# Performance work log

Hardware: AMD Instinct MI355X
Metric: run time of the kernel (lower is better)

## Reference

```python
import jax, jax.numpy as jnp
import numpy as np

B, C = 32768, 1000
ALPHA, P, BETA = 0.5, 2.0, 0.3
E1, E2 = 60, 80
MAGIC = 0.165745444183859  # constant subtracted from max_m in __init__


def setup_inputs() -> dict:
    key = jax.random.key(0)
    k1, k2, k3, k4 = jax.random.split(key, 4)
    x = jax.random.normal(k1, (B, C), dtype=jnp.float32)
    targets = jax.random.randint(k2, (B,), 0, C)
    # per-class sample counts (long-tailed): positive floats in [5, 1280]
    cls_num_list = jax.random.uniform(k3, (C,), dtype=jnp.float32, minval=5.0, maxval=1280.0)
    class_difficulty = jax.random.uniform(k4, (C,), dtype=jnp.float32)
    return {"x": x, "targets": targets, "cls_num_list": cls_num_list,
            "class_difficulty": class_difficulty, "epoch": 70}


def reference(x, targets, cls_num_list, class_difficulty, epoch):
    # ---- margins from class frequency (computed in __init__) ----
    max_m = -jnp.log(jnp.min(cls_num_list) / jnp.sum(cls_num_list)) - MAGIC
    cls_p = 1.0 / jnp.sqrt(cls_num_list)          # [C]
    m_list = max_m * cls_p / jnp.max(cls_p)       # [C]
    # ---- difficulty-based weights ----
    weights = ALPHA * class_difficulty ** P + BETA
    weights = weights * (max_m / jnp.max(weights))
    # ---- epoch schedule (epoch is a static Python int) ----
    if epoch < E1:
        m_list1 = m_list
    else:
        ee = 1.0 if epoch >= E2 else (epoch - E1) / (E2 - E1)
        m_list1 = m_list + weights * ee / 2
    # ---- subtract per-sample margin only at the target logit ----
    batch_m = m_list1[targets]                    # [B], == matmul(m_list1, onehot.T)
    rows = jnp.arange(B)
    output = x.at[rows, targets].add(-batch_m)    # torch.where(index, x - batch_m, x)
    # ---- safe_cross_entropy with s=1.0 (s kwarg not passed at call site) ----
    log_probs = jax.nn.log_softmax(output * 1.0, axis=1)
    loss = -jnp.mean(log_probs[rows, targets])
    return loss
```

## Files before the change

kernel.cpp:

```cpp
#include <hip/hip_runtime.h>
#include <math.h>

#define B_SZ 32768
#define C_SZ 1000
#define NV4  250

typedef float fvec4 __attribute__((ext_vector_type(4)));

__constant__ float kMAGIC = 0.165745444183859f;

__global__ void prep_kernel(const float* __restrict__ cls,
                            const float* __restrict__ diff,
                            const int*   __restrict__ epoch_p,
                            float*       __restrict__ m1) {
    __shared__ float smin[256], ssum[256], smax[256];
    const int tid = threadIdx.x;
    float mn = INFINITY, sm = 0.f, mx = -INFINITY;
    for (int c = tid; c < C_SZ; c += 256) {
        float v = cls[c];
        mn = fminf(mn, v);
        sm += v;
        mx = fmaxf(mx, diff[c]);
    }
    smin[tid] = mn; ssum[tid] = sm; smax[tid] = mx;
    __syncthreads();
    for (int s = 128; s > 0; s >>= 1) {
        if (tid < s) {
            smin[tid] = fminf(smin[tid], smin[tid + s]);
            ssum[tid] += ssum[tid + s];
            smax[tid] = fmaxf(smax[tid], smax[tid + s]);
        }
        __syncthreads();
    }
    __shared__ float sh_maxm, sh_minc, sh_wsc, sh_ee2;
    if (tid == 0) {
        const float minc = smin[0], sumc = ssum[0], maxd = smax[0];
        const float maxm = -logf(minc / sumc) - kMAGIC;
        const float maxw = 0.5f * maxd * maxd + 0.3f;
        const int epoch = epoch_p[0];
        float ee2;
        if (epoch < 60)       ee2 = 0.f;
        else if (epoch >= 80) ee2 = 0.5f;
        else                  ee2 = 0.5f * (float)(epoch - 60) / 20.0f;
        sh_maxm = maxm; sh_minc = minc; sh_wsc = maxm / maxw; sh_ee2 = ee2;
    }
    __syncthreads();
    const float maxm = sh_maxm, minc = sh_minc, wsc = sh_wsc, ee2 = sh_ee2;
    for (int c = tid; c < C_SZ; c += 256) {
        const float w = (0.5f * diff[c] * diff[c] + 0.3f) * wsc;
        m1[c] = maxm * sqrtf(minc / cls[c]) + w * ee2;
    }
}

__global__ __launch_bounds__(256) void loss_kernel(const float* __restrict__ x,
                                                   const int*   __restrict__ targets,
                                                   const float* __restrict__ m1,
                                                   float*       __restrict__ partials) {
    const int lane = threadIdx.x & 63;
    const int wv   = threadIdx.x >> 6;
    const int gw   = blockIdx.x * 4 + wv;
    const int nw   = gridDim.x * 4;

    float acc = 0.f;
    for (int row = gw; row < B_SZ; row += nw) {
        const fvec4* __restrict__ xr = (const fvec4*)(x + (size_t)row * C_SZ);
        const int   t  = targets[row];
        const float bm = m1[t];

        fvec4 v[4];
        #pragma unroll
        for (int k = 0; k < 4; ++k) {
            const int i4 = lane + 64 * k;
            if (i4 < NV4) v[k] = __builtin_nontemporal_load(&xr[i4]);
            else          v[k] = (fvec4){0.f, 0.f, 0.f, 0.f};
        }

        float s = 0.f;
        #pragma unroll
        for (int k = 0; k < 4; ++k) {
            const int i4   = lane + 64 * k;
            const int base = i4 * 4;
            if (i4 < NV4) {
                s += __expf(v[k].x - ((t == base + 0) ? bm : 0.f));
                s += __expf(v[k].y - ((t == base + 1) ? bm : 0.f));
                s += __expf(v[k].z - ((t == base + 2) ? bm : 0.f));
                s += __expf(v[k].w - ((t == base + 3) ? bm : 0.f));
            }
        }
        #pragma unroll
        for (int off = 32; off > 0; off >>= 1)
            s += __shfl_xor(s, off);

        const float xt = x[(size_t)row * C_SZ + t] - bm;
        acc += __logf(s) - xt;
    }

    __shared__ float sw[4];
    if (lane == 0) sw[wv] = acc;
    __syncthreads();
    if (threadIdx.x == 0)
        partials[blockIdx.x] = sw[0] + sw[1] + sw[2] + sw[3];
}

__global__ void finish_kernel(const float* __restrict__ partials, int n,
                              float* __restrict__ out) {
    __shared__ float sh[256];
    const int tid = threadIdx.x;
    float s = 0.f;
    for (int i = tid; i < n; i += 256) s += partials[i];
    sh[tid] = s;
    __syncthreads();
    for (int k = 128; k > 0; k >>= 1) {
        if (tid < k) sh[tid] += sh[tid + k];
        __syncthreads();
    }
    if (tid == 0) out[0] = sh[0] / (float)B_SZ;
}

extern "C" void kernel_launch(void* const* d_in, const int* in_sizes, int n_in,
                              void* d_out, int out_size, void* d_ws, size_t ws_size,
                              hipStream_t stream) {
    const float* x       = (const float*)d_in[0];
    const int*   targets = (const int*)d_in[1];
    const float* cls     = (const float*)d_in[2];
    const float* diff    = (const float*)d_in[3];
    const int*   epoch   = (const int*)d_in[4];
    float*       out     = (float*)d_out;

    float* m1       = (float*)d_ws;
    float* partials = m1 + C_SZ;

    prep_kernel<<<1, 256, 0, stream>>>(cls, diff, epoch, m1);

    const int grid = 2048;
    loss_kernel<<<grid, 256, 0, stream>>>(x, targets, m1, partials);

    finish_kernel<<<1, 256, 0, stream>>>(partials, grid, out);
}
```

Baseline: 194.3 us.

## Fuse margin prep into loss kernel and extract target logit from registers

Removes the single-block prep kernel by having every block of the loss kernel redundantly reduce cls/diff to compute the margin scalars, then computes each row's margin inline. The exp sum now runs over raw logits, and the target term is corrected afterwards using the target logit picked out of registers and reduced with an extra shuffle. This drops one launch and a serialized tiny kernel, plus the extra global load of x[t]. In exchange each of the 2048 blocks rereads 8 KB of class data and does a shared-memory reduction. The subtract-and-add correction of exp(xt) can also lose some float precision.

```diff
diff --git a/kernel.cpp b/kernel.cpp
--- a/kernel.cpp
+++ b/kernel.cpp
@@ -9,12 +9,15 @@
 
 __constant__ float kMAGIC = 0.165745444183859f;
 
-__global__ void prep_kernel(const float* __restrict__ cls,
-                            const float* __restrict__ diff,
-                            const int*   __restrict__ epoch_p,
-                            float*       __restrict__ m1) {
+__global__ __launch_bounds__(256) void main_kernel(const float* __restrict__ x,
+                                                   const int*   __restrict__ targets,
+                                                   const float* __restrict__ cls,
+                                                   const float* __restrict__ diff,
+                                                   const int*   __restrict__ epoch_p,
+                                                   float*       __restrict__ partials) {
     __shared__ float smin[256], ssum[256], smax[256];
     const int tid = threadIdx.x;
+
     float mn = INFINITY, sm = 0.f, mx = -INFINITY;
     for (int c = tid; c < C_SZ; c += 256) {
         float v = cls[c];
@@ -46,26 +49,16 @@
     }
     __syncthreads();
     const float maxm = sh_maxm, minc = sh_minc, wsc = sh_wsc, ee2 = sh_ee2;
-    for (int c = tid; c < C_SZ; c += 256) {
-        const float w = (0.5f * diff[c] * diff[c] + 0.3f) * wsc;
-        m1[c] = maxm * sqrtf(minc / cls[c]) + w * ee2;
-    }
-}
 
-__global__ __launch_bounds__(256) void loss_kernel(const float* __restrict__ x,
-                                                   const int*   __restrict__ targets,
-                                                   const float* __restrict__ m1,
-                                                   float*       __restrict__ partials) {
-    const int lane = threadIdx.x & 63;
-    const int wv   = threadIdx.x >> 6;
+    const int lane = tid & 63;
+    const int wv   = tid >> 6;
     const int gw   = blockIdx.x * 4 + wv;
     const int nw   = gridDim.x * 4;
 
     float acc = 0.f;
     for (int row = gw; row < B_SZ; row += nw) {
         const fvec4* __restrict__ xr = (const fvec4*)(x + (size_t)row * C_SZ);
-        const int   t  = targets[row];
-        const float bm = m1[t];
+        const int t = targets[row];
 
         fvec4 v[4];
         #pragma unroll
@@ -75,30 +68,39 @@
             else          v[k] = (fvec4){0.f, 0.f, 0.f, 0.f};
         }
 
-        float s = 0.f;
+        const float bm = maxm * sqrtf(minc / cls[t])
+                       + (0.5f * diff[t] * diff[t] + 0.3f) * wsc * ee2;
+
+        const int t4 = t >> 2, tm = t & 3;
+        float s = 0.f, xt = 0.f;
         #pragma unroll
         for (int k = 0; k < 4; ++k) {
-            const int i4   = lane + 64 * k;
-            const int base = i4 * 4;
+            const int i4 = lane + 64 * k;
             if (i4 < NV4) {
-                s += __expf(v[k].x - ((t == base + 0) ? bm : 0.f));
-                s += __expf(v[k].y - ((t == base + 1) ? bm : 0.f));
-                s += __expf(v[k].z - ((t == base + 2) ? bm : 0.f));
-                s += __expf(v[k].w - ((t == base + 3) ? bm : 0.f));
+                s += __expf(v[k].x);
+                s += __expf(v[k].y);
+                s += __expf(v[k].z);
+                s += __expf(v[k].w);
+                if (i4 == t4) {
+                    xt = (tm & 2) ? ((tm & 1) ? v[k].w : v[k].z)
+                                  : ((tm & 1) ? v[k].y : v[k].x);
+                }
             }
         }
         #pragma unroll
-        for (int off = 32; off > 0; off >>= 1)
-            s += __shfl_xor(s, off);
-
-        const float xt = x[(size_t)row * C_SZ + t] - bm;
-        acc += __logf(s) - xt;
+        for (int off = 32; off > 0; off >>= 1) {
+            s  += __shfl_xor(s,  off);
+            xt += __shfl_xor(xt, off);
+        }
+        const float xadj = xt - bm;
+        s = s - __expf(xt) + __expf(xadj);
+        acc += __logf(s) - xadj;
     }
 
     __shared__ float sw[4];
     if (lane == 0) sw[wv] = acc;
     __syncthreads();
-    if (threadIdx.x == 0)
+    if (tid == 0)
         partials[blockIdx.x] = sw[0] + sw[1] + sw[2] + sw[3];
 }
 
@@ -127,13 +129,10 @@
     const int*   epoch   = (const int*)d_in[4];
     float*       out     = (float*)d_out;
 
-    float* m1       = (float*)d_ws;
-    float* partials = m1 + C_SZ;
-
-    prep_kernel<<<1, 256, 0, stream>>>(cls, diff, epoch, m1);
+    float* partials = (float*)d_ws;
 
     const int grid = 2048;
-    loss_kernel<<<grid, 256, 0, stream>>>(x, targets, m1, partials);
+    main_kernel<<<grid, 256, 0, stream>>>(x, targets, cls, diff, epoch, partials);
 
     finish_kernel<<<1, 256, 0, stream>>>(partials, grid, out);
 }
```

Result: faster. 187.4 us (-3.6%).
